# Kernel optimization log

Measured on AMD Instinct MI355X. Metric: run time of the kernel, lower is better.

The kernel has to match this reference:

```python
import jax, jax.numpy as jnp
import numpy as np

HIDDEN = 1024
N_HEADS = 16
HEAD_DIM = HIDDEN // N_HEADS
WINDOW = 256  # symmetric window: keys j with i - W//2 <= j <= i + W//2
BATCH, SEQ = 2, 2048


def setup_inputs() -> dict:
    key = jax.random.key(0)
    ks = jax.random.split(key, 9)
    s = 0.02
    return {
        "x":  jax.random.normal(ks[0], (BATCH, SEQ, HIDDEN), dtype=jnp.float32),
        "wq": jax.random.normal(ks[1], (HIDDEN, HIDDEN), dtype=jnp.float32) * s,
        "bq": jnp.zeros((HIDDEN,), dtype=jnp.float32),
        "wk": jax.random.normal(ks[2], (HIDDEN, HIDDEN), dtype=jnp.float32) * s,
        "bk": jnp.zeros((HIDDEN,), dtype=jnp.float32),
        "wv": jax.random.normal(ks[3], (HIDDEN, HIDDEN), dtype=jnp.float32) * s,
        "bv": jnp.zeros((HIDDEN,), dtype=jnp.float32),
        "wo": jax.random.normal(ks[4], (HIDDEN, HIDDEN), dtype=jnp.float32) * s,
        "bo": jnp.zeros((HIDDEN,), dtype=jnp.float32),
    }


def reference(x, wq, bq, wk, bk, wv, bv, wo, bo):
    B, S, Hs = x.shape
    scale = HEAD_DIM ** -0.5

    def proj(w, b):
        # [B,S,Hs] -> [B,H,S,D]
        return (x @ w + b).reshape(B, S, N_HEADS, HEAD_DIM).transpose(0, 2, 1, 3)

    q = proj(wq, bq)
    k = proj(wk, bk)
    v = proj(wv, bv)

    # Clipped sliding window == band-masked full attention (identical softmax weights).
    scores = jnp.einsum('bhid,bhjd->bhij', q, k) * scale  # [B,H,S,S]
    i = jnp.arange(S)[:, None]
    j = jnp.arange(S)[None, :]
    band = (j >= i - WINDOW // 2) & (j <= i + WINDOW // 2)
    scores = jnp.where(band, scores, -jnp.inf)
    attn = jax.nn.softmax(scores, axis=-1)
    out = jnp.einsum('bhij,bhjd->bhid', attn, v)  # [B,H,S,D]
    out = out.transpose(0, 2, 1, 3).reshape(B, S, Hs)
    return out @ wo + bo
```

## Files before the change

kernel.cpp:

```cpp
#include <hip/hip_runtime.h>
#include <hip/hip_bf16.h>
#include <stdint.h>

#define BATCH 2
#define SEQ   2048
#define HID   1024
#define NH    16
#define HD    64
#define W2    128

using bhalf8 = __attribute__((ext_vector_type(8))) short;
using fvec4  = __attribute__((ext_vector_type(4))) float;
using u16x8  = __attribute__((ext_vector_type(8))) unsigned short;

__device__ __forceinline__ unsigned short f2bf(float f) {
    union { float f; unsigned int u; } c; c.f = f;
    unsigned int u = c.u;
    u += 0x7FFFu + ((u >> 16) & 1u);
    return (unsigned short)(u >> 16);
}

__device__ __forceinline__ fvec4 zero4() {
    fvec4 z = {0.f, 0.f, 0.f, 0.f};
    return z;
}

__device__ __forceinline__ void load_lds16(const void* g, void* l) {
    __builtin_amdgcn_global_load_lds(
        (const __attribute__((address_space(1))) void*)g,
        (__attribute__((address_space(3))) void*)l, 16, 0, 0);
}

__device__ __forceinline__ float rowmax16(float v) {
    v = fmaxf(v, __shfl_xor(v, 1));
    v = fmaxf(v, __shfl_xor(v, 2));
    v = fmaxf(v, __shfl_xor(v, 4));
    v = fmaxf(v, __shfl_xor(v, 8));
    return v;
}
__device__ __forceinline__ float rowsum16(float v) {
    v += __shfl_xor(v, 1);
    v += __shfl_xor(v, 2);
    v += __shfl_xor(v, 4);
    v += __shfl_xor(v, 8);
    return v;
}


__global__ __launch_bounds__(256) void k_convert_x(const float* __restrict__ x,
                                                   unsigned short* __restrict__ xb) {
    int i = (blockIdx.x * 256 + threadIdx.x) * 8;
    float4 a = *(const float4*)(x + i);
    float4 b = *(const float4*)(x + i + 4);
    u16x8 o;
    o[0] = f2bf(a.x); o[1] = f2bf(a.y); o[2] = f2bf(a.z); o[3] = f2bf(a.w);
    o[4] = f2bf(b.x); o[5] = f2bf(b.y); o[6] = f2bf(b.z); o[7] = f2bf(b.w);
    *(u16x8*)(xb + i) = o;
}

__global__ __launch_bounds__(256) void k_transpose_w(
    const float* __restrict__ w0, const float* __restrict__ w1,
    const float* __restrict__ w2, const float* __restrict__ w3,
    unsigned short* __restrict__ t0, unsigned short* __restrict__ t1,
    unsigned short* __restrict__ t2, unsigned short* __restrict__ t3) {
    int z = blockIdx.z;
    const float* src = (z == 0) ? w0 : (z == 1) ? w1 : (z == 2) ? w2 : w3;
    unsigned short* dst = (z == 0) ? t0 : (z == 1) ? t1 : (z == 2) ? t2 : t3;
    __shared__ float tile[32][33];
    int n0 = blockIdx.x * 32, k0 = blockIdx.y * 32;
    int tx = threadIdx.x, ty = threadIdx.y;
#pragma unroll
    for (int r = 0; r < 4; ++r)
        tile[ty + 8 * r][tx] = src[(size_t)(k0 + ty + 8 * r) * HID + n0 + tx];
    __syncthreads();
#pragma unroll
    for (int r = 0; r < 4; ++r)
        dst[(size_t)(n0 + ty + 8 * r) * HID + k0 + tx] = f2bf(tile[tx][ty + 8 * r]);
}


__device__ __forceinline__ void stage_tile(const unsigned short* __restrict__ A,
                                           const unsigned short* __restrict__ Bt,
                                           int m0, int n0, int k0,
                                           unsigned short* As, unsigned short* Bs,
                                           int t) {
#pragma unroll
    for (int i = 0; i < 2; ++i) {
        int slot = t + 256 * i;
        int row = slot >> 2, ch = slot & 3;
        load_lds16(A + (size_t)(m0 + row) * HID + k0 + ch * 8, As + slot * 8);
    }
#pragma unroll
    for (int i = 0; i < 2; ++i) {
        int slot = t + 256 * i;
        int row = slot >> 2, ch = slot & 3;
        load_lds16(Bt + (size_t)(n0 + row) * HID + k0 + ch * 8, Bs + slot * 8);
    }
}

__device__ __forceinline__ void gemm_tile(const unsigned short* __restrict__ A,
                                          const unsigned short* __restrict__ Bt,
                                          int m0, int n0,
                                          unsigned short (*As)[128 * 32],
                                          unsigned short (*Bs)[128 * 32],
                                          fvec4 acc[4][4]) {
    const int t = threadIdx.x;
    const int lane = t & 63;
    const int wid = t >> 6;
    const int wr = wid >> 1, wc = wid & 1;
    const int c16 = lane & 15, g = lane >> 4;

#pragma unroll
    for (int mi = 0; mi < 4; ++mi)
#pragma unroll
        for (int ni = 0; ni < 4; ++ni) acc[mi][ni] = zero4();

    stage_tile(A, Bt, m0, n0, 0, As[0], Bs[0], t);

    int cur = 0;
    for (int k0 = 0; k0 < HID; k0 += 32) {
        __syncthreads();
        if (k0 + 32 < HID)
            stage_tile(A, Bt, m0, n0, k0 + 32, As[cur ^ 1], Bs[cur ^ 1], t);

        const unsigned short* Ap = As[cur] + (wr * 64 + c16) * 32 + g * 8;
        const unsigned short* Bp = Bs[cur] + (wc * 64 + c16) * 32 + g * 8;
        bhalf8 af[4], bf[4];
#pragma unroll
        for (int i = 0; i < 4; ++i) {
            af[i] = *(const bhalf8*)(Ap + i * 16 * 32);
            bf[i] = *(const bhalf8*)(Bp + i * 16 * 32);
        }
#pragma unroll
        for (int mi = 0; mi < 4; ++mi)
#pragma unroll
            for (int ni = 0; ni < 4; ++ni)
                acc[mi][ni] = __builtin_amdgcn_mfma_f32_16x16x32_bf16(
                    af[mi], bf[ni], acc[mi][ni], 0, 0, 0);
        cur ^= 1;
    }
}

__global__ __launch_bounds__(256) void k_gemm_qkv(
    const unsigned short* __restrict__ xb,
    const unsigned short* __restrict__ wqt, const unsigned short* __restrict__ wkt,
    const unsigned short* __restrict__ wvt,
    const float* __restrict__ bq, const float* __restrict__ bk, const float* __restrict__ bv,
    unsigned short* __restrict__ qb, unsigned short* __restrict__ kbuf,
    unsigned short* __restrict__ vt) {
    __shared__ unsigned short As[2][128 * 32];
    __shared__ unsigned short Bs[2][128 * 32];
    const int z = blockIdx.z;
    const unsigned short* Bt = (z == 0) ? wqt : (z == 1) ? wkt : wvt;
    const float* bias = (z == 0) ? bq : (z == 1) ? bk : bv;
    const int m0 = blockIdx.y * 128, n0 = blockIdx.x * 128;
    fvec4 acc[4][4];
    gemm_tile(xb, Bt, m0, n0, As, Bs, acc);

    const int lane = threadIdx.x & 63, wid = threadIdx.x >> 6;
    const int wr = wid >> 1, wc = wid & 1, c16 = lane & 15, g = lane >> 4;
#pragma unroll
    for (int mi = 0; mi < 4; ++mi) {
#pragma unroll
        for (int ni = 0; ni < 4; ++ni) {
            int gcol = n0 + wc * 64 + ni * 16 + c16;
            int h = gcol >> 6, d = gcol & 63;
            float bsv = bias[gcol];
#pragma unroll
            for (int r = 0; r < 4; ++r) {
                int grow = m0 + wr * 64 + mi * 16 + 4 * g + r;
                int b = grow >> 11, s = grow & (SEQ - 1);
                float v = acc[mi][ni][r] + bsv;
                if (z == 0)
                    qb[((size_t)(b * NH + h) * SEQ + s) * HD + d] = f2bf(v * 0.125f);
                else if (z == 1)
                    kbuf[((size_t)(b * NH + h) * SEQ + s) * HD + d] = f2bf(v);
                else
                    vt[((size_t)(b * NH + h) * HD + d) * SEQ + s] = f2bf(v);
            }
        }
    }
}

__global__ __launch_bounds__(256) void k_gemm_out(
    const unsigned short* __restrict__ attn, const unsigned short* __restrict__ wot,
    const float* __restrict__ bo, float* __restrict__ out) {
    __shared__ unsigned short As[2][128 * 32];
    __shared__ unsigned short Bs[2][128 * 32];
    const int m0 = blockIdx.y * 128, n0 = blockIdx.x * 128;
    fvec4 acc[4][4];
    gemm_tile(attn, wot, m0, n0, As, Bs, acc);

    const int lane = threadIdx.x & 63, wid = threadIdx.x >> 6;
    const int wr = wid >> 1, wc = wid & 1, c16 = lane & 15, g = lane >> 4;
#pragma unroll
    for (int mi = 0; mi < 4; ++mi) {
#pragma unroll
        for (int ni = 0; ni < 4; ++ni) {
            int gcol = n0 + wc * 64 + ni * 16 + c16;
            float bsv = bo[gcol];
#pragma unroll
            for (int r = 0; r < 4; ++r) {
                int grow = m0 + wr * 64 + mi * 16 + 4 * g + r;
                out[(size_t)grow * HID + gcol] = acc[mi][ni][r] + bsv;
            }
        }
    }
}

__global__ __launch_bounds__(256) void k_attn(
    const unsigned short* __restrict__ qb, const unsigned short* __restrict__ kbuf,
    const unsigned short* __restrict__ vt, unsigned short* __restrict__ attn) {
    const int bh = blockIdx.y;
    const int wid = threadIdx.x >> 6, lane = threadIdx.x & 63;
    const int g = lane >> 4, c16 = lane & 15;
    const int q0 = blockIdx.x * 64 + wid * 16;

    const unsigned short* Qp = qb + (size_t)bh * SEQ * HD;
    const unsigned short* Kp = kbuf + (size_t)bh * SEQ * HD;
    const unsigned short* Vp = vt + (size_t)bh * HD * SEQ;

    __shared__ unsigned short Plds[4][16 * 32];
    unsigned short* myP = Plds[wid];

    bhalf8 qf0, qf1;
    {
        const unsigned short* p = Qp + (size_t)(q0 + c16) * HD + g * 8;
        qf0 = *(const bhalf8*)p;
        qf1 = *(const bhalf8*)(p + 32);
    }
    fvec4 acc[4];
#pragma unroll
    for (int i = 0; i < 4; ++i) acc[i] = zero4();
    float mrow[4] = {-1e30f, -1e30f, -1e30f, -1e30f};
    float srow[4] = {0.f, 0.f, 0.f, 0.f};

    int kstart = q0 - W2; if (kstart < 0) kstart = 0; kstart &= ~31;
    int kend = q0 + 15 + W2; if (kend > SEQ - 1) kend = SEQ - 1;

    for (int t0 = kstart; t0 <= kend; t0 += 32) {
        fvec4 sc0 = zero4(), sc1 = zero4();
        {
            const unsigned short* kp = Kp + (size_t)(t0 + c16) * HD + g * 8;
            bhalf8 ka = *(const bhalf8*)kp;
            bhalf8 kb2 = *(const bhalf8*)(kp + 32);
            sc0 = __builtin_amdgcn_mfma_f32_16x16x32_bf16(qf0, ka, sc0, 0, 0, 0);
            sc0 = __builtin_amdgcn_mfma_f32_16x16x32_bf16(qf1, kb2, sc0, 0, 0, 0);
        }
        {
            const unsigned short* kp = Kp + (size_t)(t0 + 16 + c16) * HD + g * 8;
            bhalf8 ka = *(const bhalf8*)kp;
            bhalf8 kb2 = *(const bhalf8*)(kp + 32);
            sc1 = __builtin_amdgcn_mfma_f32_16x16x32_bf16(qf0, ka, sc1, 0, 0, 0);
            sc1 = __builtin_amdgcn_mfma_f32_16x16x32_bf16(qf1, kb2, sc1, 0, 0, 0);
        }
#pragma unroll
        for (int r = 0; r < 4; ++r) {
            int ia = q0 + 4 * g + r;
            int j0 = t0 + c16, j1 = t0 + 16 + c16;
            if (j0 < ia - W2 || j0 > ia + W2) sc0[r] = -1e30f;
            if (j1 < ia - W2 || j1 > ia + W2) sc1[r] = -1e30f;
        }
#pragma unroll
        for (int r = 0; r < 4; ++r) {
            float pm = rowmax16(fmaxf(sc0[r], sc1[r]));
            float mn = fmaxf(mrow[r], pm);
            float f = __expf(mrow[r] - mn);
            mrow[r] = mn;
            float p0 = __expf(sc0[r] - mn);
            float p1 = __expf(sc1[r] - mn);
            srow[r] = srow[r] * f + (p0 + p1);
#pragma unroll
            for (int db = 0; db < 4; ++db) acc[db][r] *= f;
            myP[(4 * g + r) * 32 + c16] = f2bf(p0);
            myP[(4 * g + r) * 32 + 16 + c16] = f2bf(p1);
        }
        asm volatile("s_waitcnt lgkmcnt(0)" ::: "memory");
        __builtin_amdgcn_sched_barrier(0);
        bhalf8 pf = *(const bhalf8*)(myP + c16 * 32 + g * 8);
#pragma unroll
        for (int db = 0; db < 4; ++db) {
            const unsigned short* vp = Vp + (size_t)(db * 16 + c16) * SEQ + t0 + g * 8;
            bhalf8 vf = *(const bhalf8*)vp;
            acc[db] = __builtin_amdgcn_mfma_f32_16x16x32_bf16(pf, vf, acc[db], 0, 0, 0);
        }
    }

    float inv[4];
#pragma unroll
    for (int r = 0; r < 4; ++r) inv[r] = 1.f / rowsum16(srow[r]);

    const int b = bh >> 4, h = bh & 15;
#pragma unroll
    for (int db = 0; db < 4; ++db)
#pragma unroll
        for (int r = 0; r < 4; ++r) {
            int si = q0 + 4 * g + r;
            attn[((size_t)(b * SEQ) + si) * HID + h * HD + db * 16 + c16] =
                f2bf(acc[db][r] * inv[r]);
        }
}


extern "C" void kernel_launch(void* const* d_in, const int* in_sizes, int n_in,
                              void* d_out, int out_size, void* d_ws, size_t ws_size,
                              hipStream_t stream) {
    const float* x  = (const float*)d_in[0];
    const float* wq = (const float*)d_in[1];
    const float* bq = (const float*)d_in[2];
    const float* wk = (const float*)d_in[3];
    const float* bk = (const float*)d_in[4];
    const float* wv = (const float*)d_in[5];
    const float* bv = (const float*)d_in[6];
    const float* wo = (const float*)d_in[7];
    const float* bo = (const float*)d_in[8];
    float* out = (float*)d_out;

    char* ws = (char*)d_ws;
    unsigned short* xb   = (unsigned short*)(ws);
    unsigned short* wqt  = (unsigned short*)(ws + (8u << 20));
    unsigned short* wkt  = wqt + 1024 * 1024;
    unsigned short* wvt  = wkt + 1024 * 1024;
    unsigned short* wot  = wvt + 1024 * 1024;
    unsigned short* qb   = wot + 1024 * 1024;
    unsigned short* kbuf = qb + 4u * 1024 * 1024;
    unsigned short* vt   = kbuf + 4u * 1024 * 1024;
    unsigned short* attn = vt + 4u * 1024 * 1024;

    k_convert_x<<<dim3(2048), dim3(256), 0, stream>>>(x, xb);
    k_transpose_w<<<dim3(32, 32, 4), dim3(32, 8), 0, stream>>>(wq, wk, wv, wo,
                                                               wqt, wkt, wvt, wot);
    k_gemm_qkv<<<dim3(8, 32, 3), dim3(256), 0, stream>>>(xb, wqt, wkt, wvt,
                                                         bq, bk, bv, qb, kbuf, vt);
    k_attn<<<dim3(SEQ / 64, BATCH * NH), dim3(256), 0, stream>>>(qb, kbuf, vt, attn);
    k_gemm_out<<<dim3(8, 32), dim3(256), 0, stream>>>(attn, wot, bo, out);
}
```

Baseline: 192.1 us.

## Triple-buffer GEMM LDS staging with explicit waitcnt and XOR-swizzled layout

Moves the shared GEMM tile loop from double to triple buffering, prefetching two K-steps ahead. The generic barrier is replaced by explicit vmcnt/lgkmcnt waits plus s_barrier. The 16-byte chunk placement in LDS gets an XOR swizzle to cut bank conflicts on the MFMA fragment reads. LDS per block rises from 32KB to 48KB, which may reduce occupancy, and the hand-written waitcnt counts must match how load_lds16 is issued.

Result: no change. 189.4 us (-1.4%).

```diff
diff --git a/kernel.cpp b/kernel.cpp
--- a/kernel.cpp
+++ b/kernel.cpp
@@ -88,13 +88,9 @@
     for (int i = 0; i < 2; ++i) {
         int slot = t + 256 * i;
         int row = slot >> 2, ch = slot & 3;
-        load_lds16(A + (size_t)(m0 + row) * HID + k0 + ch * 8, As + slot * 8);
-    }
-#pragma unroll
-    for (int i = 0; i < 2; ++i) {
-        int slot = t + 256 * i;
-        int row = slot >> 2, ch = slot & 3;
-        load_lds16(Bt + (size_t)(n0 + row) * HID + k0 + ch * 8, Bs + slot * 8);
+        int chs = ch ^ ((row >> 1) & 3);
+        load_lds16(A + (size_t)(m0 + row) * HID + k0 + chs * 8, As + slot * 8);
+        load_lds16(Bt + (size_t)(n0 + row) * HID + k0 + chs * 8, Bs + slot * 8);
     }
 }
 
@@ -116,20 +112,32 @@
         for (int ni = 0; ni < 4; ++ni) acc[mi][ni] = zero4();
 
     stage_tile(A, Bt, m0, n0, 0, As[0], Bs[0], t);
-
-    int cur = 0;
+    stage_tile(A, Bt, m0, n0, 32, As[1], Bs[1], t);
+
+    int cur = 0, sb = 2;
     for (int k0 = 0; k0 < HID; k0 += 32) {
-        __syncthreads();
         if (k0 + 32 < HID)
-            stage_tile(A, Bt, m0, n0, k0 + 32, As[cur ^ 1], Bs[cur ^ 1], t);
-
-        const unsigned short* Ap = As[cur] + (wr * 64 + c16) * 32 + g * 8;
-        const unsigned short* Bp = Bs[cur] + (wc * 64 + c16) * 32 + g * 8;
+            asm volatile("s_waitcnt vmcnt(4)" ::: "memory");
+        else
+            asm volatile("s_waitcnt vmcnt(0)" ::: "memory");
+        asm volatile("s_waitcnt lgkmcnt(0)" ::: "memory");
+        __builtin_amdgcn_sched_barrier(0);
+        __builtin_amdgcn_s_barrier();
+
+        if (k0 + 64 < HID) {
+            stage_tile(A, Bt, m0, n0, k0 + 64, As[sb], Bs[sb], t);
+            sb = (sb == 2) ? 0 : sb + 1;
+        }
+
+        const unsigned short* Ab = As[cur];
+        const unsigned short* Bb = Bs[cur];
         bhalf8 af[4], bf[4];
 #pragma unroll
         for (int i = 0; i < 4; ++i) {
-            af[i] = *(const bhalf8*)(Ap + i * 16 * 32);
-            bf[i] = *(const bhalf8*)(Bp + i * 16 * 32);
+            int ra = wr * 64 + i * 16 + c16;
+            int rb = wc * 64 + i * 16 + c16;
+            af[i] = *(const bhalf8*)(Ab + ra * 32 + (g ^ ((ra >> 1) & 3)) * 8);
+            bf[i] = *(const bhalf8*)(Bb + rb * 32 + (g ^ ((rb >> 1) & 3)) * 8);
         }
 #pragma unroll
         for (int mi = 0; mi < 4; ++mi)
@@ -137,7 +145,7 @@
             for (int ni = 0; ni < 4; ++ni)
                 acc[mi][ni] = __builtin_amdgcn_mfma_f32_16x16x32_bf16(
                     af[mi], bf[ni], acc[mi][ni], 0, 0, 0);
-        cur ^= 1;
+        cur = (cur == 2) ? 0 : cur + 1;
     }
 }
 
@@ -148,8 +156,8 @@
     const float* __restrict__ bq, const float* __restrict__ bk, const float* __restrict__ bv,
     unsigned short* __restrict__ qb, unsigned short* __restrict__ kbuf,
     unsigned short* __restrict__ vt) {
-    __shared__ unsigned short As[2][128 * 32];
-    __shared__ unsigned short Bs[2][128 * 32];
+    __shared__ unsigned short As[3][128 * 32];
+    __shared__ unsigned short Bs[3][128 * 32];
     const int z = blockIdx.z;
     const unsigned short* Bt = (z == 0) ? wqt : (z == 1) ? wkt : wvt;
     const float* bias = (z == 0) ? bq : (z == 1) ? bk : bv;
@@ -185,8 +193,8 @@
 __global__ __launch_bounds__(256) void k_gemm_out(
     const unsigned short* __restrict__ attn, const unsigned short* __restrict__ wot,
     const float* __restrict__ bo, float* __restrict__ out) {
-    __shared__ unsigned short As[2][128 * 32];
-    __shared__ unsigned short Bs[2][128 * 32];
+    __shared__ unsigned short As[3][128 * 32];
+    __shared__ unsigned short Bs[3][128 * 32];
     const int m0 = blockIdx.y * 128, n0 = blockIdx.x * 128;
     fvec4 acc[4][4];
     gemm_tile(attn, wot, m0, n0, As, Bs, acc);
```
